# Kernel optimization log

Hardware: AMD Instinct MI355X
Metric: run time of the kernel (lower is better)

Reference implementation:

```python
import jax, jax.numpy as jnp
import numpy as np

K_CLS, M_PROTO, C = 19, 10, 720
EPS_SK, SK_ITERS = 0.05, 3  # standard distributed_sinkhorn defaults (SwAV/ProtoSeg)


def _layernorm(x, g, b, eps=1e-5):
    mu = jnp.mean(x, axis=-1, keepdims=True)
    var = jnp.var(x, axis=-1, keepdims=True)
    return (x - mu) * jax.lax.rsqrt(var + eps) * g + b


def _l2n(x):
    return x / jnp.clip(jnp.linalg.norm(x, axis=-1, keepdims=True), 1e-12, None)


def _masked_sinkhorn(scores, mask):
    # scores: [K, N, M] per-class similarity; mask: [K, N] (1.0 where gt_seg == class k)
    # Faithful to distributed_sinkhorn(init_q) run per class, vectorized over classes
    # with masking instead of data-dependent boolean gather (jit-safe).
    L = jnp.exp(scores / EPS_SK) * mask[..., None]                     # [K, N, M]
    L = L / jnp.clip(jnp.sum(L, axis=(1, 2), keepdims=True), 1e-12, None)
    n = jnp.sum(mask, axis=1)[:, None, None]                           # pixels per class [K,1,1]
    n_safe = jnp.maximum(n, 1.0)

    def body(L, _):
        # normalize each prototype row (sum over pixels), then divide by M
        L = L / jnp.clip(jnp.sum(L, axis=1, keepdims=True), 1e-12, None) / M_PROTO
        # normalize each pixel column (sum over prototypes), then divide by n
        L = L / jnp.clip(jnp.sum(L, axis=2, keepdims=True), 1e-12, None) / n_safe
        L = L * mask[..., None]
        return L, None

    L, _ = jax.lax.scan(body, L, None, length=SK_ITERS)
    return L * n_safe                                                  # [K, N, M]


def setup_inputs() -> dict:
    key = jax.random.key(0)
    k1, k2, k3 = jax.random.split(key, 3)
    N = 4 * 128 * 128  # batch 4, 512x512 crop at HRNet output stride 4
    return {
        "x": jax.random.normal(k1, (N, C), jnp.float32),
        "gt_seg": jax.random.randint(k2, (N,), 0, K_CLS),
        "feat_gamma": jnp.ones((C,), jnp.float32),
        "feat_beta": jnp.zeros((C,), jnp.float32),
        "prototypes": jax.random.normal(k3, (K_CLS, M_PROTO, C), jnp.float32) * 0.02,
    }


def reference(x, gt_seg, feat_gamma, feat_beta, prototypes):
    # similarity_compute (cosine branch)
    xn = _l2n(_layernorm(x, feat_gamma, feat_beta))                    # [N, C]
    protos = _l2n(prototypes)                                          # [K, M, C]
    sim_mat = jnp.einsum('nd,kmd->nmk', xn, protos)                    # [N, M, K]

    # prototype_learning
    s = jnp.max(sim_mat, axis=1)                                       # amax over prototypes -> [N, K]
    pred_seg = jnp.argmax(s, axis=-1)                                  # [N]
    scores = jnp.transpose(sim_mat, (2, 0, 1))                         # [K, N, M]
    mask = jnp.transpose(jax.nn.one_hot(gt_seg, K_CLS, dtype=sim_mat.dtype))  # [K, N]
    q = _masked_sinkhorn(scores, mask)                                 # [K, N, M]
    return sim_mat, q, pred_seg
```

## Files before the change

kernel.cpp:

```cpp
#include <hip/hip_runtime.h>
#include <stdint.h>

#define N_PIX    65536
#define C_DIM    720
#define K_CLS    19
#define M_PROTO  10
#define NPROTO   190
#define CPAD     768
#define OFF_Q    12451840
#define OFF_PRED 24903680

typedef _Float16 half8 __attribute__((ext_vector_type(8)));
typedef _Float16 h4    __attribute__((ext_vector_type(4)));
typedef float    f32x4 __attribute__((ext_vector_type(4)));

#define WS_E       0u
#define WS_G2      768u
#define WS_G3      1536u
#define WS_CNT     2304u
#define WS_TIECNT  2432u
#define WS_PSCALE  4096u
#define WS_EPIX    1052672u
#define WS_U       3674112u
#define WS_TIELIST 3936256u
#define WS_PF16    4198400u
#define WS_PF32    4493312u

__device__ __forceinline__ void async16(const void* g, void* l) {
    __builtin_amdgcn_global_load_lds(
        (const __attribute__((address_space(1))) unsigned int*)g,
        (__attribute__((address_space(3))) unsigned int*)l, 16, 0, 0);
}

__global__ void proto_prep(const float* __restrict__ protos,
                           _Float16* __restrict__ pf16,
                           float* __restrict__ pf32,
                           float* __restrict__ wsf) {
    int p = blockIdx.x;
    int tid = threadIdx.x;
    if (p >= NPROTO) {
        for (int c = tid; c < CPAD; c += 256) pf16[(size_t)p * CPAD + c] = (_Float16)0.f;
        if (p == 191) for (int i = tid; i < 640; i += 256) wsf[i] = 0.f;
        return;
    }
    __shared__ float red[256];
    const float* row = protos + (size_t)p * C_DIM;
    float ss = 0.f;
    for (int c = tid; c < C_DIM; c += 256) { float v = row[c]; ss += v * v; }
    red[tid] = ss;
    __syncthreads();
    for (int s = 128; s > 0; s >>= 1) {
        if (tid < s) red[tid] += red[tid + s];
        __syncthreads();
    }
    float invn = 1.f / fmaxf(sqrtf(red[0]), 1e-12f);
    int e8 = p & 7;
    for (int c = tid; c < CPAD; c += 256) {
        float v = (c < C_DIM) ? row[c] * invn : 0.f;
        int sw = (((c >> 3) ^ e8) << 3) | (c & 7);
        pf16[(size_t)p * CPAD + sw] = (_Float16)v;
        if (c < C_DIM) pf32[(size_t)p * C_DIM + c] = v;
    }
}

__global__ __launch_bounds__(256, 2) void gemm_fused(
        const float*  __restrict__ x,
        const float*  __restrict__ gamma,
        const float*  __restrict__ beta,
        const _Float16* __restrict__ pf16,
        const int*    __restrict__ gt_seg,
        float4* __restrict__ pscale,
        float* __restrict__ out_sim,
        float* __restrict__ out_pred,
        float* __restrict__ epix,
        float* __restrict__ E,
        float* __restrict__ cnt,
        int*   __restrict__ tiecnt,
        int*   __restrict__ tielist) {
    extern __shared__ __align__(16) char smem[];
    _Float16* xt = (_Float16*)smem;
    _Float16* ps = (_Float16*)(smem + 49152);

    int tid = threadIdx.x;
    int wave = tid >> 6, lane = tid & 63;
    int lane15 = lane & 15, quad = lane >> 4;
    int n0 = blockIdx.x * 32;
    int rsub = lane >> 3, csub = (lane & 7) << 3;

    const float4* g4 = (const float4*)gamma;
    const float4* b4 = (const float4*)beta;
    float4 gv[3], bv[3];
    #pragma unroll
    for (int j = 0; j < 3; ++j) {
        int f = lane + 64 * j;
        float4 z = make_float4(0.f, 0.f, 0.f, 0.f);
        gv[j] = (f < 180) ? g4[f] : z;
        bv[j] = (f < 180) ? b4[f] : z;
    }
    float4 xv[8][3];
    #pragma unroll
    for (int rr = 0; rr < 8; ++rr) {
        int row = wave * 8 + rr;
        const float4* row4 = (const float4*)(x + (size_t)(n0 + row) * C_DIM);
        #pragma unroll
        for (int j = 0; j < 3; ++j) {
            int f = lane + 64 * j;
            float4 z = make_float4(0.f, 0.f, 0.f, 0.f);
            xv[rr][j] = (f < 180) ? row4[f] : z;
        }
    }
    #pragma unroll
    for (int rr = 0; rr < 8; ++rr) {
        int row = wave * 8 + rr;
        int n = n0 + row;
        float a[8];
        #pragma unroll
        for (int t = 0; t < 8; ++t) a[t] = 0.f;
        #pragma unroll
        for (int j = 0; j < 3; ++j) {
            float4 xvv = xv[rr][j], gvv = gv[j], bvv = bv[j];
            #define ACC1(v, g, b) { float g2 = (g)*(g); a[0] += (v); a[1] += (v)*(v); \
                a[2] += (v)*g2; a[3] += (v)*(v)*g2; a[4] += (v)*(g)*(b); a[5] += g2; \
                a[6] += (g)*(b); a[7] += (b)*(b); }
            ACC1(xvv.x, gvv.x, bvv.x); ACC1(xvv.y, gvv.y, bvv.y);
            ACC1(xvv.z, gvv.z, bvv.z); ACC1(xvv.w, gvv.w, bvv.w);
            #undef ACC1
        }
        #pragma unroll
        for (int m = 1; m < 64; m <<= 1) {
            #pragma unroll
            for (int t = 0; t < 8; ++t) a[t] += __shfl_xor(a[t], m);
        }
        float mu   = a[0] * (1.f / 720.f);
        float var  = a[1] * (1.f / 720.f) - mu * mu;
        float rsig = rsqrtf(var + 1e-5f);
        float ny2  = rsig * rsig * (a[3] - 2.f * mu * a[2] + mu * mu * a[5])
                   + 2.f * rsig * (a[4] - mu * a[6]) + a[7];
        float rn   = 1.f / fmaxf(sqrtf(fmaxf(ny2, 0.f)), 1e-12f);
        float pp   = rsig * rn;
        float qq   = -pp * mu;
        if (lane == 0) pscale[n] = make_float4(pp, qq, rn, 0.f);
        #pragma unroll
        for (int j = 0; j < 3; ++j) {
            int f = lane + 64 * j;
            float4 xvv = xv[rr][j], gvv = gv[j], bvv = bv[j];
            h4 o;
            o.x = (_Float16)((pp * xvv.x + qq) * gvv.x + rn * bvv.x);
            o.y = (_Float16)((pp * xvv.y + qq) * gvv.y + rn * bvv.y);
            o.z = (_Float16)((pp * xvv.z + qq) * gvv.z + rn * bvv.z);
            o.w = (_Float16)((pp * xvv.w + qq) * gvv.w + rn * bvv.w);
            int gl = f >> 1;
            int gp = (gl & 0x78) | ((gl ^ row) & 7);
            *reinterpret_cast<h4*>(xt + row * 768 + gp * 8 + (f & 1) * 4) = o;
        }
    }
    __syncthreads();

    _Float16* myps = ps + wave * (48 * 64);
    f32x4 acc[2][3];
    #pragma unroll
    for (int pt = 0; pt < 2; ++pt)
        #pragma unroll
        for (int ct = 0; ct < 3; ++ct) acc[pt][ct] = (f32x4){0.f, 0.f, 0.f, 0.f};

    int e8 = lane15 & 7;
    #pragma unroll 1
    for (int ch = 0; ch < 12; ++ch) {
        #pragma unroll
        for (int i = 0; i < 6; ++i) {
            const _Float16* g = pf16 + (size_t)(wave * 48 + i * 8 + rsub) * CPAD + ch * 64 + csub;
            async16(g, myps + i * 8 * 64);
        }
        asm volatile("s_waitcnt vmcnt(0)" ::: "memory");
        __builtin_amdgcn_sched_barrier(0);
        #pragma unroll
        for (int ks = 0; ks < 2; ++ks) {
            int s = (ks * 4 + quad) ^ e8;
            half8 a0 = *reinterpret_cast<const half8*>(xt + (lane15) * 768 + (ch * 8 + s) * 8);
            half8 a1 = *reinterpret_cast<const half8*>(xt + (16 + lane15) * 768 + (ch * 8 + s) * 8);
            half8 b[3];
            #pragma unroll
            for (int ct = 0; ct < 3; ++ct)
                b[ct] = *reinterpret_cast<const half8*>(myps + (ct * 16 + lane15) * 64 + s * 8);
            #pragma unroll
            for (int ct = 0; ct < 3; ++ct) {
                acc[0][ct] = __builtin_amdgcn_mfma_f32_16x16x32_f16(a0, b[ct], acc[0][ct], 0, 0, 0);
                acc[1][ct] = __builtin_amdgcn_mfma_f32_16x16x32_f16(a1, b[ct], acc[1][ct], 0, 0, 0);
            }
        }
        asm volatile("s_waitcnt lgkmcnt(0)" ::: "memory");
        __builtin_amdgcn_sched_barrier(0);
    }

    __syncthreads();
    float* fsm   = (float*)smem;
    float* ebuf  = fsm;
    float* smaxs = fsm + 6400;
    float* Eks   = fsm + 7008;
    float* hist  = fsm + 7200;
    if (tid < 224) fsm[7008 + tid] = 0.f;
    #pragma unroll
    for (int pt = 0; pt < 2; ++pt) {
        #pragma unroll
        for (int ct = 0; ct < 3; ++ct) {
            int proto = wave * 48 + ct * 16 + lane15;
            if (proto < NPROTO) {
                int kc = proto / 10;
                int m = proto - kc * 10;
                int ob = m * 19 + kc;
                int prow = pt * 16 + quad * 4;
                #pragma unroll
                for (int r = 0; r < 4; ++r)
                    ebuf[(prow + r) * 200 + ob] = acc[pt][ct][r];
            }
        }
    }
    __syncthreads();
    for (int t2 = tid; t2 < 32 * 192; t2 += 256) {
        int p = t2 / 192, col = t2 - p * 192;
        if (col < NPROTO)
            out_sim[(size_t)(n0 + p) * 190 + col] = ebuf[p * 200 + col];
    }
    for (int t2 = tid; t2 < 608; t2 += 256) {
        int p = t2 / 19, k = t2 - p * 19;
        const float* rowp = ebuf + p * 200;
        float mx = rowp[k];
        #pragma unroll
        for (int m = 1; m < 10; ++m) mx = fmaxf(mx, rowp[m * 19 + k]);
        smaxs[t2] = mx;
    }
    __syncthreads();
    if (tid < 32) {
        int p = tid;
        int pixel = n0 + p;
        float best = smaxs[p * 19], second = -1e30f;
        int bk = 0;
        #pragma unroll
        for (int k = 1; k < 19; ++k) {
            float v = smaxs[p * 19 + k];
            if (v > best) { second = best; best = v; bk = k; }
            else if (v > second) second = v;
        }
        out_pred[pixel] = (float)bk;
        if (best - second < 3e-4f) {
            int pos = atomicAdd(tiecnt, 1);
            if (pos < N_PIX) tielist[pos] = pixel;
        }
        int g = gt_seg[pixel];
        atomicAdd(&hist[g], 1.f);
        const float* rowp = ebuf + p * 200;
        #pragma unroll
        for (int m = 0; m < 10; ++m) {
            float ev = __expf(rowp[m * 19 + g] * 20.f);
            epix[(size_t)pixel * 10 + m] = ev;
            atomicAdd(&Eks[g * 10 + m], ev);
        }
    }
    __syncthreads();
    if (tid < 190) atomicAdd(&E[tid], Eks[tid]);
    if (tid < 19)  atomicAdd(&cnt[tid], hist[tid]);
}

__global__ void tiefix(const float* __restrict__ x,
                       const float4* __restrict__ pscale,
                       const float* __restrict__ gamma,
                       const float* __restrict__ beta,
                       const float* __restrict__ pf32,
                       const int* __restrict__ tiecnt,
                       const int* __restrict__ tielist,
                       float* __restrict__ out_pred) {
    __shared__ float xrow[720];
    __shared__ double sd[190];
    int count = *tiecnt;
    if (count > N_PIX) count = N_PIX;
    int wave = threadIdx.x >> 6, lane = threadIdx.x & 63;
    for (int it = blockIdx.x; it < count; it += gridDim.x) {
        int n = tielist[it];
        float4 sc = pscale[n];
        for (int c = threadIdx.x; c < 720; c += 256)
            xrow[c] = (sc.x * x[(size_t)n * 720 + c] + sc.y) * gamma[c] + sc.z * beta[c];
        __syncthreads();
        for (int p = wave; p < NPROTO; p += 4) {
            const float* pr = pf32 + (size_t)p * 720;
            double a = 0.0;
            for (int j = 0; j < 12; ++j) {
                int i = lane + 64 * j;
                if (i < 720) a += (double)xrow[i] * (double)pr[i];
            }
            #pragma unroll
            for (int m = 1; m < 64; m <<= 1) a += __shfl_xor(a, m);
            if (lane == 0) sd[p] = a;
        }
        __syncthreads();
        if (threadIdx.x == 0) {
            double best = -1e300;
            int bk = 0;
            for (int k = 0; k < 19; ++k) {
                double sk = -1e300;
                for (int m = 0; m < 10; ++m) sk = fmax(sk, sd[k * 10 + m]);
                if (sk > best) { best = sk; bk = k; }
            }
            out_pred[n] = (float)bk;
        }
        __syncthreads();
    }
}

__global__ void pk_fused(const float* __restrict__ epix,
                         const int* __restrict__ gt_seg,
                         const float* __restrict__ E,
                         const float* __restrict__ Gprev,
                         const float* __restrict__ cnt,
                         const float* __restrict__ uin,
                         float* __restrict__ uout,
                         float* __restrict__ Gout) {
    __shared__ float Es[190];
    __shared__ float vs[190];
    __shared__ float cs[19];
    __shared__ float Ga[190];
    int tid = threadIdx.x;
    if (tid < 190) { Es[tid] = E[tid]; Ga[tid] = 0.f; }
    if (tid < 19) cs[tid] = cnt[tid];
    __syncthreads();
    if (tid < 190) {
        int k = tid / 10;
        float S = 0.f;
        #pragma unroll
        for (int m = 0; m < 10; ++m) S += Es[k * 10 + m];
        float v0 = 1.f / fmaxf(S, 1e-12f);
        float vv = v0 / (fmaxf(v0 * Es[tid], 1e-12f) * 10.f);
        if (Gprev) vv = vv / (fmaxf(vv * Gprev[tid], 1e-12f) * 10.f);
        vs[tid] = vv;
    }
    __syncthreads();
    int n = blockIdx.x * 256 + tid;
    int g = gt_seg[n];
    float ns = fmaxf(cs[g], 1.f);
    const float* e = epix + (size_t)n * 10;
    float ev[10];
    float dot = 0.f;
    #pragma unroll
    for (int m = 0; m < 10; ++m) { ev[m] = e[m]; dot += ev[m] * vs[g * 10 + m]; }
    float up = uin ? uin[n] : 1.f;
    float c = up * dot;
    float uu = up / (fmaxf(c, 1e-12f) * ns);
    uout[n] = uu;
    #pragma unroll
    for (int m = 0; m < 10; ++m) atomicAdd(&Ga[g * 10 + m], ev[m] * uu);
    __syncthreads();
    if (tid < 190) atomicAdd(&Gout[tid], Ga[tid]);
}

__global__ void p3k_fused(const float* __restrict__ epix,
                          const int* __restrict__ gt_seg,
                          const float* __restrict__ E,
                          const float* __restrict__ G2,
                          const float* __restrict__ G3,
                          const float* __restrict__ cnt,
                          const float* __restrict__ uin,
                          float* __restrict__ qout) {
    __shared__ float Es[190];
    __shared__ float vs[190];
    __shared__ float cs[19];
    int tid = threadIdx.x;
    if (tid < 190) Es[tid] = E[tid];
    if (tid < 19) cs[tid] = cnt[tid];
    __syncthreads();
    if (tid < 190) {
        int k = tid / 10;
        float S = 0.f;
        #pragma unroll
        for (int m = 0; m < 10; ++m) S += Es[k * 10 + m];
        float v0 = 1.f / fmaxf(S, 1e-12f);
        float vv = v0 / (fmaxf(v0 * Es[tid], 1e-12f) * 10.f);
        vv = vv / (fmaxf(vv * G2[tid], 1e-12f) * 10.f);
        vv = vv / (fmaxf(vv * G3[tid], 1e-12f) * 10.f);
        vs[tid] = vv;
    }
    __syncthreads();
    int n = blockIdx.x * 256 + tid;
    int g = gt_seg[n];
    float ns = fmaxf(cs[g], 1.f);
    const float* e = epix + (size_t)n * 10;
    float ev[10];
    float dot = 0.f;
    #pragma unroll
    for (int m = 0; m < 10; ++m) { ev[m] = e[m]; dot += ev[m] * vs[g * 10 + m]; }
    float up = uin[n];
    float c = up * dot;
    float u3 = up / (fmaxf(c, 1e-12f) * ns);
    float2 qv[5];
    #pragma unroll
    for (int j = 0; j < 5; ++j) {
        qv[j].x = ev[2 * j] * u3 * vs[g * 10 + 2 * j] * ns;
        qv[j].y = ev[2 * j + 1] * u3 * vs[g * 10 + 2 * j + 1] * ns;
    }
    const float2 z2 = make_float2(0.f, 0.f);
    for (int k = 0; k < 19; ++k) {
        float2* dst = reinterpret_cast<float2*>(qout + (size_t)k * 655360 + (size_t)n * 10);
        if (k == g) {
            #pragma unroll
            for (int j = 0; j < 5; ++j) dst[j] = qv[j];
        } else {
            #pragma unroll
            for (int j = 0; j < 5; ++j) dst[j] = z2;
        }
    }
}

extern "C" void kernel_launch(void* const* d_in, const int* in_sizes, int n_in,
                              void* d_out, int out_size, void* d_ws, size_t ws_size,
                              hipStream_t stream) {
    const float* x      = (const float*)d_in[0];
    const int*   gt     = (const int*)d_in[1];
    const float* gamma  = (const float*)d_in[2];
    const float* beta   = (const float*)d_in[3];
    const float* protos = (const float*)d_in[4];
    float* out = (float*)d_out;
    char* ws = (char*)d_ws;

    float*  E       = (float*)(ws + WS_E);
    float*  G2      = (float*)(ws + WS_G2);
    float*  G3      = (float*)(ws + WS_G3);
    float*  cnt     = (float*)(ws + WS_CNT);
    int*    tiecnt  = (int*)(ws + WS_TIECNT);
    float4* pscale  = (float4*)(ws + WS_PSCALE);
    float*  epix    = (float*)(ws + WS_EPIX);
    float*  u       = (float*)(ws + WS_U);
    int*    tielist = (int*)(ws + WS_TIELIST);
    _Float16* pf16  = (_Float16*)(ws + WS_PF16);
    float*  pf32    = (float*)(ws + WS_PF32);

    static bool attr_set = false;
    if (!attr_set) {
        hipFuncSetAttribute((const void*)gemm_fused,
                            hipFuncAttributeMaxDynamicSharedMemorySize, 73728);
        attr_set = true;
    }

    proto_prep<<<192, 256, 0, stream>>>(protos, pf16, pf32, (float*)ws);
    gemm_fused<<<2048, 256, 73728, stream>>>(x, gamma, beta, pf16, gt, pscale,
                                             out, out + OFF_PRED, epix, E, cnt,
                                             tiecnt, tielist);
    tiefix<<<1024, 256, 0, stream>>>(x, pscale, gamma, beta, pf32, tiecnt, tielist, out + OFF_PRED);
    pk_fused<<<256, 256, 0, stream>>>(epix, gt, E, nullptr, cnt, nullptr, u, G2);
    pk_fused<<<256, 256, 0, stream>>>(epix, gt, E, G2, cnt, u, u, G3);
    p3k_fused<<<256, 256, 0, stream>>>(epix, gt, E, G2, G3, cnt, u, out + OFF_Q);
}
```

Before: 483.1 us.

## Load prototype fragments directly from global, shrink LDS and raise occupancy

The GEMM stage now reads the normalized prototype operand straight from global memory (L2) into registers instead of staging it through LDS with async loads. This drops the prototype swizzle, cuts dynamic shared memory to 48KB and raises launch bounds to 3 blocks per CU, aiming for better latency hiding. It also hoists the gamma/beta-only sums out of the per-row reduction, shortening the shuffle chain. The per-pixel exp and atomics epilogue is spread over 320 threads instead of 32. The trade-off is more global/L2 traffic for B and tighter register limits that may cause spills.

After: 482.7 us. No clear change (-0.1%).

```diff
diff --git a/kernel.cpp b/kernel.cpp
--- a/kernel.cpp
+++ b/kernel.cpp
@@ -26,12 +26,6 @@
 #define WS_PF16    4198400u
 #define WS_PF32    4493312u
 
-__device__ __forceinline__ void async16(const void* g, void* l) {
-    __builtin_amdgcn_global_load_lds(
-        (const __attribute__((address_space(1))) unsigned int*)g,
-        (__attribute__((address_space(3))) unsigned int*)l, 16, 0, 0);
-}
-
 __global__ void proto_prep(const float* __restrict__ protos,
                            _Float16* __restrict__ pf16,
                            float* __restrict__ pf32,
@@ -54,16 +48,14 @@
         __syncthreads();
     }
     float invn = 1.f / fmaxf(sqrtf(red[0]), 1e-12f);
-    int e8 = p & 7;
     for (int c = tid; c < CPAD; c += 256) {
         float v = (c < C_DIM) ? row[c] * invn : 0.f;
-        int sw = (((c >> 3) ^ e8) << 3) | (c & 7);
-        pf16[(size_t)p * CPAD + sw] = (_Float16)v;
+        pf16[(size_t)p * CPAD + c] = (_Float16)v;
         if (c < C_DIM) pf32[(size_t)p * C_DIM + c] = v;
     }
 }
 
-__global__ __launch_bounds__(256, 2) void gemm_fused(
+__global__ __launch_bounds__(256, 3) void gemm_fused(
         const float*  __restrict__ x,
         const float*  __restrict__ gamma,
         const float*  __restrict__ beta,
@@ -79,13 +71,11 @@
         int*   __restrict__ tielist) {
     extern __shared__ __align__(16) char smem[];
     _Float16* xt = (_Float16*)smem;
-    _Float16* ps = (_Float16*)(smem + 49152);
 
     int tid = threadIdx.x;
     int wave = tid >> 6, lane = tid & 63;
     int lane15 = lane & 15, quad = lane >> 4;
     int n0 = blockIdx.x * 32;
-    int rsub = lane >> 3, csub = (lane & 7) << 3;
 
     const float4* g4 = (const float4*)gamma;
     const float4* b4 = (const float4*)beta;
@@ -97,6 +87,20 @@
         gv[j] = (f < 180) ? g4[f] : z;
         bv[j] = (f < 180) ? b4[f] : z;
     }
+    float s5 = 0.f, s6 = 0.f, s7 = 0.f;
+    #pragma unroll
+    for (int j = 0; j < 3; ++j) {
+        float4 g = gv[j], b = bv[j];
+        s5 += g.x * g.x; s6 += g.x * b.x; s7 += b.x * b.x;
+        s5 += g.y * g.y; s6 += g.y * b.y; s7 += b.y * b.y;
+        s5 += g.z * g.z; s6 += g.z * b.z; s7 += b.z * b.z;
+        s5 += g.w * g.w; s6 += g.w * b.w; s7 += b.w * b.w;
+    }
+    #pragma unroll
+    for (int m = 1; m < 64; m <<= 1) {
+        s5 += __shfl_xor(s5, m); s6 += __shfl_xor(s6, m); s7 += __shfl_xor(s7, m);
+    }
+
     float4 xv[8][3];
     #pragma unroll
     for (int rr = 0; rr < 8; ++rr) {
@@ -113,29 +117,27 @@
     for (int rr = 0; rr < 8; ++rr) {
         int row = wave * 8 + rr;
         int n = n0 + row;
-        float a[8];
-        #pragma unroll
-        for (int t = 0; t < 8; ++t) a[t] = 0.f;
+        float a0 = 0.f, a1 = 0.f, a2 = 0.f, a3 = 0.f, a4 = 0.f;
         #pragma unroll
         for (int j = 0; j < 3; ++j) {
             float4 xvv = xv[rr][j], gvv = gv[j], bvv = bv[j];
-            #define ACC1(v, g, b) { float g2 = (g)*(g); a[0] += (v); a[1] += (v)*(v); \
-                a[2] += (v)*g2; a[3] += (v)*(v)*g2; a[4] += (v)*(g)*(b); a[5] += g2; \
-                a[6] += (g)*(b); a[7] += (b)*(b); }
+            #define ACC1(v, g, b) { float g2 = (g)*(g); a0 += (v); a1 += (v)*(v); \
+                a2 += (v)*g2; a3 += (v)*(v)*g2; a4 += (v)*(g)*(b); }
             ACC1(xvv.x, gvv.x, bvv.x); ACC1(xvv.y, gvv.y, bvv.y);
             ACC1(xvv.z, gvv.z, bvv.z); ACC1(xvv.w, gvv.w, bvv.w);
             #undef ACC1
         }
         #pragma unroll
         for (int m = 1; m < 64; m <<= 1) {
-            #pragma unroll
-            for (int t = 0; t < 8; ++t) a[t] += __shfl_xor(a[t], m);
-        }
-        float mu   = a[0] * (1.f / 720.f);
-        float var  = a[1] * (1.f / 720.f) - mu * mu;
+            a0 += __shfl_xor(a0, m); a1 += __shfl_xor(a1, m);
+            a2 += __shfl_xor(a2, m); a3 += __shfl_xor(a3, m);
+            a4 += __shfl_xor(a4, m);
+        }
+        float mu   = a0 * (1.f / 720.f);
+        float var  = a1 * (1.f / 720.f) - mu * mu;
         float rsig = rsqrtf(var + 1e-5f);
-        float ny2  = rsig * rsig * (a[3] - 2.f * mu * a[2] + mu * mu * a[5])
-                   + 2.f * rsig * (a[4] - mu * a[6]) + a[7];
+        float ny2  = rsig * rsig * (a3 - 2.f * mu * a2 + mu * mu * s5)
+                   + 2.f * rsig * (a4 - mu * s6) + s7;
         float rn   = 1.f / fmaxf(sqrtf(fmaxf(ny2, 0.f)), 1e-12f);
         float pp   = rsig * rn;
         float qq   = -pp * mu;
@@ -156,7 +158,6 @@
     }
     __syncthreads();
 
-    _Float16* myps = ps + wave * (48 * 64);
     f32x4 acc[2][3];
     #pragma unroll
     for (int pt = 0; pt < 2; ++pt)
@@ -164,32 +165,26 @@
         for (int ct = 0; ct < 3; ++ct) acc[pt][ct] = (f32x4){0.f, 0.f, 0.f, 0.f};
 
     int e8 = lane15 & 7;
-    #pragma unroll 1
+    const _Float16* pb0 = pf16 + (size_t)(wave * 48 + lane15) * CPAD + quad * 8;
+    #pragma unroll 2
     for (int ch = 0; ch < 12; ++ch) {
-        #pragma unroll
-        for (int i = 0; i < 6; ++i) {
-            const _Float16* g = pf16 + (size_t)(wave * 48 + i * 8 + rsub) * CPAD + ch * 64 + csub;
-            async16(g, myps + i * 8 * 64);
-        }
-        asm volatile("s_waitcnt vmcnt(0)" ::: "memory");
-        __builtin_amdgcn_sched_barrier(0);
+        half8 b[2][3];
+        #pragma unroll
+        for (int ks = 0; ks < 2; ++ks)
+            #pragma unroll
+            for (int ct = 0; ct < 3; ++ct)
+                b[ks][ct] = *reinterpret_cast<const half8*>(pb0 + ct * 16 * CPAD + ch * 64 + ks * 32);
         #pragma unroll
         for (int ks = 0; ks < 2; ++ks) {
             int s = (ks * 4 + quad) ^ e8;
-            half8 a0 = *reinterpret_cast<const half8*>(xt + (lane15) * 768 + (ch * 8 + s) * 8);
+            half8 a0 = *reinterpret_cast<const half8*>(xt + lane15 * 768 + (ch * 8 + s) * 8);
             half8 a1 = *reinterpret_cast<const half8*>(xt + (16 + lane15) * 768 + (ch * 8 + s) * 8);
-            half8 b[3];
-            #pragma unroll
-            for (int ct = 0; ct < 3; ++ct)
-                b[ct] = *reinterpret_cast<const half8*>(myps + (ct * 16 + lane15) * 64 + s * 8);
             #pragma unroll
             for (int ct = 0; ct < 3; ++ct) {
-                acc[0][ct] = __builtin_amdgcn_mfma_f32_16x16x32_f16(a0, b[ct], acc[0][ct], 0, 0, 0);
-                acc[1][ct] = __builtin_amdgcn_mfma_f32_16x16x32_f16(a1, b[ct], acc[1][ct], 0, 0, 0);
+                acc[0][ct] = __builtin_amdgcn_mfma_f32_16x16x32_f16(a0, b[ks][ct], acc[0][ct], 0, 0, 0);
+                acc[1][ct] = __builtin_amdgcn_mfma_f32_16x16x32_f16(a1, b[ks][ct], acc[1][ct], 0, 0, 0);
             }
         }
-        asm volatile("s_waitcnt lgkmcnt(0)" ::: "memory");
-        __builtin_amdgcn_sched_barrier(0);
     }
 
     __syncthreads();
@@ -198,7 +193,9 @@
     float* smaxs = fsm + 6400;
     float* Eks   = fsm + 7008;
     float* hist  = fsm + 7200;
+    int*   gts   = (int*)(fsm + 7232);
     if (tid < 224) fsm[7008 + tid] = 0.f;
+    if (tid < 32) gts[tid] = gt_seg[n0 + tid];
     #pragma unroll
     for (int pt = 0; pt < 2; ++pt) {
         #pragma unroll
@@ -229,6 +226,14 @@
         for (int m = 1; m < 10; ++m) mx = fmaxf(mx, rowp[m * 19 + k]);
         smaxs[t2] = mx;
     }
+    for (int t2 = tid; t2 < 320; t2 += 256) {
+        int p = t2 / 10, m = t2 - p * 10;
+        int g = gts[p];
+        float ev = __expf(ebuf[p * 200 + m * 19 + g] * 20.f);
+        epix[(size_t)(n0 + p) * 10 + m] = ev;
+        atomicAdd(&Eks[g * 10 + m], ev);
+        if (m == 0) atomicAdd(&hist[g], 1.f);
+    }
     __syncthreads();
     if (tid < 32) {
         int p = tid;
@@ -246,17 +251,7 @@
             int pos = atomicAdd(tiecnt, 1);
             if (pos < N_PIX) tielist[pos] = pixel;
         }
-        int g = gt_seg[pixel];
-        atomicAdd(&hist[g], 1.f);
-        const float* rowp = ebuf + p * 200;
-        #pragma unroll
-        for (int m = 0; m < 10; ++m) {
-            float ev = __expf(rowp[m * 19 + g] * 20.f);
-            epix[(size_t)pixel * 10 + m] = ev;
-            atomicAdd(&Eks[g * 10 + m], ev);
-        }
-    }
-    __syncthreads();
+    }
     if (tid < 190) atomicAdd(&E[tid], Eks[tid]);
     if (tid < 19)  atomicAdd(&cnt[tid], hist[tid]);
 }
@@ -434,12 +429,12 @@
     static bool attr_set = false;
     if (!attr_set) {
         hipFuncSetAttribute((const void*)gemm_fused,
-                            hipFuncAttributeMaxDynamicSharedMemorySize, 73728);
+                            hipFuncAttributeMaxDynamicSharedMemorySize, 49152);
         attr_set = true;
     }
 
     proto_prep<<<192, 256, 0, stream>>>(protos, pf16, pf32, (float*)ws);
-    gemm_fused<<<2048, 256, 73728, stream>>>(x, gamma, beta, pf16, gt, pscale,
+    gemm_fused<<<2048, 256, 49152, stream>>>(x, gamma, beta, pf16, gt, pscale,
                                              out, out + OFF_PRED, epix, E, cnt,
                                              tiecnt, tielist);
     tiefix<<<1024, 256, 0, stream>>>(x, pscale, gamma, beta, pf32, tiecnt, tielist, out + OFF_PRED);
```
